# Kernel tuning notes

Measured on AMD Instinct MI355X. Metric: run time of the kernel, lower is better.

Reference implementation:

```python
import jax, jax.numpy as jnp
import numpy as np

DIM = 1024

def setup_inputs() -> dict:
    key = jax.random.key(0)
    ks = jax.random.split(key, 8)
    B, Sx, Sy, D = 4, 2048, 2048, DIM
    s = 1.0 / np.sqrt(D)
    return {
        "x": jax.random.normal(ks[0], (B, Sx, D), jnp.float32),
        "y": jax.random.normal(ks[1], (B, Sy, D), jnp.float32),
        "Wq": jax.random.normal(ks[2], (D, D), jnp.float32) * s,
        "bq": jnp.zeros((D,), jnp.float32),
        "Wk": jax.random.normal(ks[3], (D, D), jnp.float32) * s,
        "bk": jnp.zeros((D,), jnp.float32),
        "Wv": jax.random.normal(ks[4], (D, D), jnp.float32) * s,
        "bv": jnp.zeros((D,), jnp.float32),
    }

def reference(x, y, Wq, bq, Wk, bk, Wv, bv):
    D = x.shape[-1]
    scale = jnp.sqrt(jnp.asarray(D, x.dtype))
    Q = jnp.einsum('bsd,de->bse', x, Wq) + bq  # [B,Sx,D]
    K = jnp.einsum('btd,de->bte', y, Wk) + bk  # [B,Sy,D]
    V = jnp.einsum('btd,de->bte', y, Wv) + bv  # [B,Sy,D]
    scores = jnp.einsum('bse,bte->bst', Q, K) / scale  # [B,Sx,Sy]
    probs = jax.nn.softmax(scores, axis=-1)
    out = jnp.einsum('bst,bte->bse', probs, V)  # [B,Sx,D]
    return out
```

## Files before the change

### kernel.cpp

```cpp
#include <hip/hip_runtime.h>

typedef __bf16 bf16x8_t __attribute__((ext_vector_type(8)));
typedef float f32x4_t __attribute__((ext_vector_type(4)));
typedef unsigned short ushort_t;

__device__ __forceinline__ unsigned short f2bf(float f) {
  unsigned u = __float_as_uint(f);
  u = (u + 0x7FFFu + ((u >> 16) & 1u)) >> 16;
  return (unsigned short)u;
}
__device__ __forceinline__ float bf2f(unsigned short h) {
  return __uint_as_float(((unsigned)h) << 16);
}

__device__ __forceinline__ void gload16(const void* g, void* l) {
  __builtin_amdgcn_global_load_lds(
      (const __attribute__((address_space(1))) unsigned int*)g,
      (__attribute__((address_space(3))) unsigned int*)l, 16, 0, 0);
}

template<bool OUT_BF16, bool HAS_BIAS>
__global__ __launch_bounds__(256, 3)
void gemm_nt(const ushort_t* __restrict__ A, const ushort_t* __restrict__ Bt,
             void* __restrict__ Cp, const float* __restrict__ bias,
             int gx, int gy, int K, int lda, int ldb, int ldc,
             long sA, long sB, long sC, float alpha)
{
  __shared__ __align__(16) ushort_t smem[2][8192];
  const int tid = threadIdx.x;
  const int lane = tid & 63;
  const int wave = tid >> 6;

  const int per = gridDim.x >> 3;
  int wg = blockIdx.x;
  wg = (wg & 7) * per + (wg >> 3);
  const int bz = wg / (gx * gy);
  const int rr = wg - bz * gx * gy;
  const int by = rr / gx, bx = rr - by * gx;
  const int bm = by * 128, bn = bx * 128;

  const ushort_t* Ab = A + (long)bz * sA;
  const ushort_t* Bb = Bt + (long)bz * sB;

  const int r_s0 = wave * 16 + (lane >> 2);
  const int r_s1 = (wave + 4) * 16 + (lane >> 2);
  const int c_s0 = (((lane & 3) ^ ((r_s0 >> 1) & 3)) << 3);
  const int c_s1 = (((lane & 3) ^ ((r_s1 >> 1) & 3)) << 3);
  const ushort_t* gA0 = Ab + (long)(bm + r_s0) * lda + c_s0;
  const ushort_t* gA1 = Ab + (long)(bm + r_s1) * lda + c_s1;
  const ushort_t* gB0 = Bb + (long)(bn + r_s0) * ldb + c_s0;
  const ushort_t* gB1 = Bb + (long)(bn + r_s1) * ldb + c_s1;

  auto stage = [&](int kt, int buf) {
    const int k0 = kt << 5;
    ushort_t* s = smem[buf];
    gload16(gA0 + k0, s + wave * 512);
    gload16(gA1 + k0, s + (wave + 4) * 512);
    gload16(gB0 + k0, s + 4096 + wave * 512);
    gload16(gB1 + k0, s + 4096 + (wave + 4) * 512);
  };

  const int wr = wave >> 1, wc = wave & 1;
  int offA[4], offB[4];
#pragma unroll
  for (int m = 0; m < 4; ++m) {
    const int row = wr * 64 + m * 16 + (lane & 15);
    offA[m] = row * 32 + ((((lane >> 4) ^ ((row >> 1) & 3))) << 3);
  }
#pragma unroll
  for (int n = 0; n < 4; ++n) {
    const int row = wc * 64 + n * 16 + (lane & 15);
    offB[n] = 4096 + row * 32 + ((((lane >> 4) ^ ((row >> 1) & 3))) << 3);
  }

  f32x4_t acc[4][4];
  const f32x4_t z4 = {0.f, 0.f, 0.f, 0.f};
#pragma unroll
  for (int m = 0; m < 4; ++m)
#pragma unroll
    for (int n = 0; n < 4; ++n) acc[m][n] = z4;

  stage(0, 0);
  __syncthreads();

  const int nt = K >> 5;
  for (int kt = 0; kt < nt; ++kt) {
    const int cur = kt & 1;
    if (kt + 1 < nt) stage(kt + 1, cur ^ 1);
    const ushort_t* s = smem[cur];
    bf16x8_t af[4], bfv[4];
#pragma unroll
    for (int m = 0; m < 4; ++m)
      af[m] = __builtin_bit_cast(bf16x8_t, *(const uint4*)(s + offA[m]));
#pragma unroll
    for (int n = 0; n < 4; ++n)
      bfv[n] = __builtin_bit_cast(bf16x8_t, *(const uint4*)(s + offB[n]));
#pragma unroll
    for (int m = 0; m < 4; ++m)
#pragma unroll
      for (int n = 0; n < 4; ++n)
        acc[m][n] = __builtin_amdgcn_mfma_f32_16x16x32_bf16(af[m], bfv[n], acc[m][n], 0, 0, 0);
    __syncthreads();
  }

  const long zC = (long)bz * sC;
  const int r0 = (lane >> 4) * 4;
  const int c0 = lane & 15;
#pragma unroll
  for (int m = 0; m < 4; ++m) {
    const int grow0 = bm + wr * 64 + m * 16 + r0;
#pragma unroll
    for (int n = 0; n < 4; ++n) {
      const int gcol = bn + wc * 64 + n * 16 + c0;
      float bv_ = 0.f;
      if constexpr (HAS_BIAS) bv_ = bias[gcol];
#pragma unroll
      for (int i = 0; i < 4; ++i) {
        const float v = acc[m][n][i] * alpha + bv_;
        if constexpr (OUT_BF16) {
          ((ushort_t*)Cp)[zC + (long)(grow0 + i) * ldc + gcol] = f2bf(v);
        } else {
          ((float*)Cp)[zC + (long)(grow0 + i) * ldc + gcol] = v;
        }
      }
    }
  }
}

__global__ __launch_bounds__(256)
void conv_f32_bf16(const float* __restrict__ in, ushort_t* __restrict__ out) {
  const long i = (long)blockIdx.x * 256 + threadIdx.x;
  const float4 a = ((const float4*)in)[i * 2];
  const float4 b = ((const float4*)in)[i * 2 + 1];
  uint4 o;
  o.x = (unsigned)f2bf(a.x) | ((unsigned)f2bf(a.y) << 16);
  o.y = (unsigned)f2bf(a.z) | ((unsigned)f2bf(a.w) << 16);
  o.z = (unsigned)f2bf(b.x) | ((unsigned)f2bf(b.y) << 16);
  o.w = (unsigned)f2bf(b.z) | ((unsigned)f2bf(b.w) << 16);
  ((uint4*)out)[i] = o;
}

__global__ __launch_bounds__(256)
void wtrans(const float* __restrict__ W, ushort_t* __restrict__ Wt) {
  __shared__ float tile[32][33];
  const int bx = blockIdx.x * 32;
  const int by = blockIdx.y * 32;
  const int t = threadIdx.x;
  const int c = t & 31, r0 = t >> 5;
#pragma unroll
  for (int i = 0; i < 4; ++i)
    tile[r0 + i * 8][c] = W[(long)(by + r0 + i * 8) * 1024 + bx + c];
  __syncthreads();
#pragma unroll
  for (int i = 0; i < 4; ++i)
    Wt[(long)(bx + r0 + i * 8) * 1024 + by + c] = f2bf(tile[c][r0 + i * 8]);
}

__global__ __launch_bounds__(256)
void transpose_bf16(const ushort_t* __restrict__ in, ushort_t* __restrict__ out,
                    int rows, int cols) {
  __shared__ ushort_t t[64][65];
  in += (long)blockIdx.z * rows * cols;
  out += (long)blockIdx.z * rows * cols;
  const int r0 = blockIdx.y * 64, c0 = blockIdx.x * 64;
  const int tc = threadIdx.x & 31;
  const int tr = threadIdx.x >> 5;
#pragma unroll
  for (int i = 0; i < 8; ++i) {
    const unsigned v = *(const unsigned*)(in + (long)(r0 + tr + 8 * i) * cols + c0 + tc * 2);
    t[tr + 8 * i][tc * 2] = (ushort_t)(v & 0xffff);
    t[tr + 8 * i][tc * 2 + 1] = (ushort_t)(v >> 16);
  }
  __syncthreads();
#pragma unroll
  for (int i = 0; i < 8; ++i) {
    const unsigned v = (unsigned)t[tc * 2][tr + 8 * i] |
                       ((unsigned)t[tc * 2 + 1][tr + 8 * i] << 16);
    *(unsigned*)(out + (long)(c0 + tr + 8 * i) * rows + r0 + tc * 2) = v;
  }
}

__global__ __launch_bounds__(256)
void softmax_rows(ushort_t* __restrict__ S) {
  const long row = blockIdx.x;
  ushort_t* p = S + row * 2048;
  const int t = threadIdx.x;
  uint4 v = ((uint4*)p)[t];
  ushort_t* hp = (ushort_t*)&v;
  float f[8];
#pragma unroll
  for (int j = 0; j < 8; ++j) f[j] = bf2f(hp[j]);

  float m = f[0];
#pragma unroll
  for (int j = 1; j < 8; ++j) m = fmaxf(m, f[j]);
#pragma unroll
  for (int s = 32; s; s >>= 1) m = fmaxf(m, __shfl_xor(m, s, 64));
  __shared__ float redm[4];
  __shared__ float reds[4];
  const int wave = t >> 6, lane = t & 63;
  if (lane == 0) redm[wave] = m;
  __syncthreads();
  m = fmaxf(fmaxf(redm[0], redm[1]), fmaxf(redm[2], redm[3]));

  float sum = 0.f;
#pragma unroll
  for (int j = 0; j < 8; ++j) { f[j] = __expf(f[j] - m); sum += f[j]; }
#pragma unroll
  for (int s = 32; s; s >>= 1) sum += __shfl_xor(sum, s, 64);
  if (lane == 0) reds[wave] = sum;
  __syncthreads();
  sum = reds[0] + reds[1] + reds[2] + reds[3];
  const float inv = 1.0f / sum;
#pragma unroll
  for (int j = 0; j < 8; ++j) hp[j] = f2bf(f[j] * inv);
  ((uint4*)p)[t] = v;
}

extern "C" void kernel_launch(void* const* d_in, const int* in_sizes, int n_in,
                              void* d_out, int out_size, void* d_ws, size_t ws_size,
                              hipStream_t stream) {
  const float* x  = (const float*)d_in[0];
  const float* y  = (const float*)d_in[1];
  const float* Wq = (const float*)d_in[2];
  const float* bq = (const float*)d_in[3];
  const float* Wk = (const float*)d_in[4];
  const float* bk = (const float*)d_in[5];
  const float* Wv = (const float*)d_in[6];
  const float* bv = (const float*)d_in[7];
  float* out = (float*)d_out;

  const int B = 4, Sx = 2048, Sy = 2048, D = 1024;
  const long M = (long)B * Sx;

  ushort_t* ws  = (ushort_t*)d_ws;
  ushort_t* Wqt = ws;
  ushort_t* Wkt = Wqt + (1u << 20);
  ushort_t* Wvt = Wkt + (1u << 20);
  ushort_t* Qb  = Wvt + (1u << 20);
  ushort_t* Kb  = Qb + (8u << 20);
  ushort_t* Sb  = Kb + (8u << 20);
  ushort_t* xb  = Sb + (16u << 20);
  ushort_t* yb  = xb + (8u << 20);
  ushort_t* Vn  = Sb;
  ushort_t* Vt  = xb;

  dim3 blk(256);

  conv_f32_bf16<<<dim3(4096), blk, 0, stream>>>(x, xb);
  conv_f32_bf16<<<dim3(4096), blk, 0, stream>>>(y, yb);
  wtrans<<<dim3(32, 32), blk, 0, stream>>>(Wq, Wqt);
  wtrans<<<dim3(32, 32), blk, 0, stream>>>(Wk, Wkt);
  wtrans<<<dim3(32, 32), blk, 0, stream>>>(Wv, Wvt);

  gemm_nt<true, true><<<dim3(512), blk, 0, stream>>>(
      xb, Wqt, Qb, bq, 8, 64, D, D, D, D, 0, 0, 0, 1.0f);
  gemm_nt<true, true><<<dim3(512), blk, 0, stream>>>(
      yb, Wkt, Kb, bk, 8, 64, D, D, D, D, 0, 0, 0, 1.0f);
  gemm_nt<true, true><<<dim3(512), blk, 0, stream>>>(
      yb, Wvt, Vn, bv, 8, 64, D, D, D, D, 0, 0, 0, 1.0f);
  transpose_bf16<<<dim3(16, 32, 4), blk, 0, stream>>>(Vn, Vt, Sy, D);

  gemm_nt<true, false><<<dim3(1024), blk, 0, stream>>>(
      Qb, Kb, Sb, nullptr, 16, 16, D, D, D, Sy,
      (long)Sx * D, (long)Sy * D, (long)Sx * Sy, 0.03125f);

  softmax_rows<<<dim3(B * Sx), blk, 0, stream>>>(Sb);

  gemm_nt<false, false><<<dim3(512), blk, 0, stream>>>(
      Sb, Vt, out, nullptr, 8, 16, Sy, Sy, Sy, D,
      (long)Sx * Sy, (long)D * Sy, (long)Sx * D, 1.0f);
}
```

Measured before the change: 208.3 us.

## Switch GEMMs to 32x32x16 MFMA, fuse K/V projection, batch prep kernels

The GEMM kernel now uses 32x32x16 bf16 MFMA with 2x2 accumulator tiles per wave in place of 4x4 tiles of 16x16x32, with a matching LDS swizzle and a launch bound of 4. The K and V projections become one GEMM over concatenated weights and biases, writing interleaved KV rows, so y is read once. The f32-to-bf16 conversion and the three weight transposes are merged into single launches. The goal is fewer LDS reads per MFMA and fewer kernel launches. The cost is a strided epilogue layout and an extra small bias-concat kernel.

After: 217.3 us. 4.3% more time.

```diff
diff --git a/kernel.cpp b/kernel.cpp
--- a/kernel.cpp
+++ b/kernel.cpp
@@ -1,7 +1,7 @@
 #include <hip/hip_runtime.h>
 
 typedef __bf16 bf16x8_t __attribute__((ext_vector_type(8)));
-typedef float f32x4_t __attribute__((ext_vector_type(4)));
+typedef float f32x16_t __attribute__((ext_vector_type(16)));
 typedef unsigned short ushort_t;
 
 __device__ __forceinline__ unsigned short f2bf(float f) {
@@ -20,16 +20,17 @@
 }
 
 template<bool OUT_BF16, bool HAS_BIAS>
-__global__ __launch_bounds__(256, 3)
-void gemm_nt(const ushort_t* __restrict__ A, const ushort_t* __restrict__ Bt,
-             void* __restrict__ Cp, const float* __restrict__ bias,
-             int gx, int gy, int K, int lda, int ldb, int ldc,
-             long sA, long sB, long sC, float alpha)
+__global__ __launch_bounds__(256, 4)
+void gemm32(const ushort_t* __restrict__ A, const ushort_t* __restrict__ Bt,
+            void* __restrict__ Cp, const float* __restrict__ bias,
+            int gx, int gy, int K, int lda, int ldb, int ldc,
+            long sA, long sB, long sC, float alpha)
 {
-  __shared__ __align__(16) ushort_t smem[2][8192];
+  __shared__ __align__(16) ushort_t sm[16384];
   const int tid = threadIdx.x;
   const int lane = tid & 63;
-  const int wave = tid >> 6;
+  const int w = tid >> 6;
+  const int wr = w >> 1, wc = w & 1;
 
   const int per = gridDim.x >> 3;
   int wg = blockIdx.x;
@@ -39,88 +40,94 @@
   const int by = rr / gx, bx = rr - by * gx;
   const int bm = by * 128, bn = bx * 128;
 
-  const ushort_t* Ab = A + (long)bz * sA;
-  const ushort_t* Bb = Bt + (long)bz * sB;
-
-  const int r_s0 = wave * 16 + (lane >> 2);
-  const int r_s1 = (wave + 4) * 16 + (lane >> 2);
-  const int c_s0 = (((lane & 3) ^ ((r_s0 >> 1) & 3)) << 3);
-  const int c_s1 = (((lane & 3) ^ ((r_s1 >> 1) & 3)) << 3);
-  const ushort_t* gA0 = Ab + (long)(bm + r_s0) * lda + c_s0;
-  const ushort_t* gA1 = Ab + (long)(bm + r_s1) * lda + c_s1;
-  const ushort_t* gB0 = Bb + (long)(bn + r_s0) * ldb + c_s0;
-  const ushort_t* gB1 = Bb + (long)(bn + r_s1) * ldb + c_s1;
+  const int r0 = (w * 2) * 16 + (lane >> 2);
+  const int csw = (((lane & 3) ^ (r0 & 3)) << 3);
+  const ushort_t* pA0 = A + (long)bz * sA + (long)(bm + r0) * lda + csw;
+  const ushort_t* pA1 = pA0 + 16 * lda;
+  const ushort_t* pB0 = Bt + (long)bz * sB + (long)(bn + r0) * ldb + csw;
+  const ushort_t* pB1 = pB0 + 16 * ldb;
 
   auto stage = [&](int kt, int buf) {
     const int k0 = kt << 5;
-    ushort_t* s = smem[buf];
-    gload16(gA0 + k0, s + wave * 512);
-    gload16(gA1 + k0, s + (wave + 4) * 512);
-    gload16(gB0 + k0, s + 4096 + wave * 512);
-    gload16(gB1 + k0, s + 4096 + (wave + 4) * 512);
+    ushort_t* s = sm + buf * 8192;
+    gload16(pA0 + k0, s + (w * 2) * 512);
+    gload16(pA1 + k0, s + (w * 2 + 1) * 512);
+    gload16(pB0 + k0, s + 4096 + (w * 2) * 512);
+    gload16(pB1 + k0, s + 4096 + (w * 2 + 1) * 512);
   };
 
-  const int wr = wave >> 1, wc = wave & 1;
-  int offA[4], offB[4];
-#pragma unroll
-  for (int m = 0; m < 4; ++m) {
-    const int row = wr * 64 + m * 16 + (lane & 15);
-    offA[m] = row * 32 + ((((lane >> 4) ^ ((row >> 1) & 3))) << 3);
-  }
-#pragma unroll
-  for (int n = 0; n < 4; ++n) {
-    const int row = wc * 64 + n * 16 + (lane & 15);
-    offB[n] = 4096 + row * 32 + ((((lane >> 4) ^ ((row >> 1) & 3))) << 3);
-  }
-
-  f32x4_t acc[4][4];
-  const f32x4_t z4 = {0.f, 0.f, 0.f, 0.f};
-#pragma unroll
-  for (int m = 0; m < 4; ++m)
-#pragma unroll
-    for (int n = 0; n < 4; ++n) acc[m][n] = z4;
+  const int l31 = lane & 31, kh = lane >> 5;
+  int offA[2][2], offB[2][2];
+#pragma unroll
+  for (int m = 0; m < 2; ++m) {
+    const int row = wr * 64 + m * 32 + l31;
+#pragma unroll
+    for (int s = 0; s < 2; ++s)
+      offA[m][s] = row * 32 + (((s * 2 + kh) ^ (row & 3)) << 3);
+  }
+#pragma unroll
+  for (int n = 0; n < 2; ++n) {
+    const int row = wc * 64 + n * 32 + l31;
+#pragma unroll
+    for (int s = 0; s < 2; ++s)
+      offB[n][s] = 4096 + row * 32 + (((s * 2 + kh) ^ (row & 3)) << 3);
+  }
+
+  f32x16_t acc[2][2];
+#pragma unroll
+  for (int m = 0; m < 2; ++m)
+#pragma unroll
+    for (int n = 0; n < 2; ++n)
+#pragma unroll
+      for (int i = 0; i < 16; ++i) acc[m][n][i] = 0.f;
 
   stage(0, 0);
   __syncthreads();
 
+#define LDX(off) __builtin_bit_cast(bf16x8_t, *(const uint4*)(sp + (off)))
   const int nt = K >> 5;
   for (int kt = 0; kt < nt; ++kt) {
     const int cur = kt & 1;
     if (kt + 1 < nt) stage(kt + 1, cur ^ 1);
-    const ushort_t* s = smem[cur];
-    bf16x8_t af[4], bfv[4];
-#pragma unroll
-    for (int m = 0; m < 4; ++m)
-      af[m] = __builtin_bit_cast(bf16x8_t, *(const uint4*)(s + offA[m]));
-#pragma unroll
-    for (int n = 0; n < 4; ++n)
-      bfv[n] = __builtin_bit_cast(bf16x8_t, *(const uint4*)(s + offB[n]));
-#pragma unroll
-    for (int m = 0; m < 4; ++m)
-#pragma unroll
-      for (int n = 0; n < 4; ++n)
-        acc[m][n] = __builtin_amdgcn_mfma_f32_16x16x32_bf16(af[m], bfv[n], acc[m][n], 0, 0, 0);
+    const ushort_t* sp = sm + cur * 8192;
+    bf16x8_t af[2][2], bf[2][2];
+#pragma unroll
+    for (int m = 0; m < 2; ++m)
+#pragma unroll
+      for (int s = 0; s < 2; ++s) af[m][s] = LDX(offA[m][s]);
+#pragma unroll
+    for (int n = 0; n < 2; ++n)
+#pragma unroll
+      for (int s = 0; s < 2; ++s) bf[n][s] = LDX(offB[n][s]);
+#pragma unroll
+    for (int s = 0; s < 2; ++s)
+#pragma unroll
+      for (int m = 0; m < 2; ++m)
+#pragma unroll
+        for (int n = 0; n < 2; ++n)
+          acc[m][n] = __builtin_amdgcn_mfma_f32_32x32x16_bf16(
+              af[m][s], bf[n][s], acc[m][n], 0, 0, 0);
     __syncthreads();
   }
+#undef LDX
 
   const long zC = (long)bz * sC;
-  const int r0 = (lane >> 4) * 4;
-  const int c0 = lane & 15;
-#pragma unroll
-  for (int m = 0; m < 4; ++m) {
-    const int grow0 = bm + wr * 64 + m * 16 + r0;
-#pragma unroll
-    for (int n = 0; n < 4; ++n) {
-      const int gcol = bn + wc * 64 + n * 16 + c0;
+#pragma unroll
+  for (int m = 0; m < 2; ++m) {
+    const int growb = bm + wr * 64 + m * 32;
+#pragma unroll
+    for (int n = 0; n < 2; ++n) {
+      const int gcol = bn + wc * 64 + n * 32 + l31;
       float bv_ = 0.f;
       if constexpr (HAS_BIAS) bv_ = bias[gcol];
 #pragma unroll
-      for (int i = 0; i < 4; ++i) {
-        const float v = acc[m][n][i] * alpha + bv_;
+      for (int r = 0; r < 16; ++r) {
+        const int grow = growb + (r & 3) + 8 * (r >> 2) + 4 * kh;
+        const float v = acc[m][n][r] * alpha + bv_;
         if constexpr (OUT_BF16) {
-          ((ushort_t*)Cp)[zC + (long)(grow0 + i) * ldc + gcol] = f2bf(v);
+          ((ushort_t*)Cp)[zC + (long)grow * ldc + gcol] = f2bf(v);
         } else {
-          ((float*)Cp)[zC + (long)(grow0 + i) * ldc + gcol] = v;
+          ((float*)Cp)[zC + (long)grow * ldc + gcol] = v;
         }
       }
     }
@@ -128,20 +135,28 @@
 }
 
 __global__ __launch_bounds__(256)
-void conv_f32_bf16(const float* __restrict__ in, ushort_t* __restrict__ out) {
-  const long i = (long)blockIdx.x * 256 + threadIdx.x;
+void conv2(const float* __restrict__ x, const float* __restrict__ y,
+           ushort_t* __restrict__ xb, ushort_t* __restrict__ yb) {
+  const int b = blockIdx.x;
+  const float* in = (b < 4096) ? x : y;
+  ushort_t* out = (b < 4096) ? xb : yb;
+  const long i = (long)(b & 4095) * 256 + threadIdx.x;
   const float4 a = ((const float4*)in)[i * 2];
-  const float4 b = ((const float4*)in)[i * 2 + 1];
+  const float4 c = ((const float4*)in)[i * 2 + 1];
   uint4 o;
   o.x = (unsigned)f2bf(a.x) | ((unsigned)f2bf(a.y) << 16);
   o.y = (unsigned)f2bf(a.z) | ((unsigned)f2bf(a.w) << 16);
-  o.z = (unsigned)f2bf(b.x) | ((unsigned)f2bf(b.y) << 16);
-  o.w = (unsigned)f2bf(b.z) | ((unsigned)f2bf(b.w) << 16);
+  o.z = (unsigned)f2bf(c.x) | ((unsigned)f2bf(c.y) << 16);
+  o.w = (unsigned)f2bf(c.z) | ((unsigned)f2bf(c.w) << 16);
   ((uint4*)out)[i] = o;
 }
 
 __global__ __launch_bounds__(256)
-void wtrans(const float* __restrict__ W, ushort_t* __restrict__ Wt) {
+void wtrans3(const float* __restrict__ W0, const float* __restrict__ W1,
+             const float* __restrict__ W2, ushort_t* __restrict__ T0,
+             ushort_t* __restrict__ T1, ushort_t* __restrict__ T2) {
+  const float* W = (blockIdx.z == 0) ? W0 : (blockIdx.z == 1) ? W1 : W2;
+  ushort_t* Wt = (blockIdx.z == 0) ? T0 : (blockIdx.z == 1) ? T1 : T2;
   __shared__ float tile[32][33];
   const int bx = blockIdx.x * 32;
   const int by = blockIdx.y * 32;
@@ -157,26 +172,33 @@
 }
 
 __global__ __launch_bounds__(256)
+void bconcat(const float* __restrict__ a, const float* __restrict__ b,
+             float* __restrict__ o) {
+  const int i = blockIdx.x * 256 + threadIdx.x;
+  o[i] = (i < 1024) ? a[i] : b[i - 1024];
+}
+
+__global__ __launch_bounds__(256)
 void transpose_bf16(const ushort_t* __restrict__ in, ushort_t* __restrict__ out,
-                    int rows, int cols) {
-  __shared__ ushort_t t[64][65];
-  in += (long)blockIdx.z * rows * cols;
-  out += (long)blockIdx.z * rows * cols;
+                    int ld_in, int ld_out, long in_bs, long out_bs) {
+  __shared__ ushort_t tt[64][65];
+  in += (long)blockIdx.z * in_bs;
+  out += (long)blockIdx.z * out_bs;
   const int r0 = blockIdx.y * 64, c0 = blockIdx.x * 64;
   const int tc = threadIdx.x & 31;
   const int tr = threadIdx.x >> 5;
 #pragma unroll
   for (int i = 0; i < 8; ++i) {
-    const unsigned v = *(const unsigned*)(in + (long)(r0 + tr + 8 * i) * cols + c0 + tc * 2);
-    t[tr + 8 * i][tc * 2] = (ushort_t)(v & 0xffff);
-    t[tr + 8 * i][tc * 2 + 1] = (ushort_t)(v >> 16);
+    const unsigned v = *(const unsigned*)(in + (long)(r0 + tr + 8 * i) * ld_in + c0 + tc * 2);
+    tt[tr + 8 * i][tc * 2] = (ushort_t)(v & 0xffff);
+    tt[tr + 8 * i][tc * 2 + 1] = (ushort_t)(v >> 16);
   }
   __syncthreads();
 #pragma unroll
   for (int i = 0; i < 8; ++i) {
-    const unsigned v = (unsigned)t[tc * 2][tr + 8 * i] |
-                       ((unsigned)t[tc * 2 + 1][tr + 8 * i] << 16);
-    *(unsigned*)(out + (long)(c0 + tr + 8 * i) * rows + r0 + tc * 2) = v;
+    const unsigned v = (unsigned)tt[tc * 2][tr + 8 * i] |
+                       ((unsigned)tt[tc * 2 + 1][tr + 8 * i] << 16);
+    *(unsigned*)(out + (long)(c0 + tr + 8 * i) * ld_out + r0 + tc * 2) = v;
   }
 }
 
@@ -230,44 +252,41 @@
   const float* bv = (const float*)d_in[7];
   float* out = (float*)d_out;
 
-  const int B = 4, Sx = 2048, Sy = 2048, D = 1024;
-  const long M = (long)B * Sx;
+  const int D = 1024;
+  const long MB_ = 1l << 20;
 
   ushort_t* ws  = (ushort_t*)d_ws;
   ushort_t* Wqt = ws;
-  ushort_t* Wkt = Wqt + (1u << 20);
-  ushort_t* Wvt = Wkt + (1u << 20);
-  ushort_t* Qb  = Wvt + (1u << 20);
-  ushort_t* Kb  = Qb + (8u << 20);
-  ushort_t* Sb  = Kb + (8u << 20);
-  ushort_t* xb  = Sb + (16u << 20);
-  ushort_t* yb  = xb + (8u << 20);
-  ushort_t* Vn  = Sb;
-  ushort_t* Vt  = xb;
+  ushort_t* Wkv = ws + 1 * MB_;
+  ushort_t* Wvt = ws + 2 * MB_;
+  ushort_t* Qb  = ws + 3 * MB_;
+  ushort_t* KV  = ws + 11 * MB_;
+  ushort_t* yb  = ws + 27 * MB_;
+  ushort_t* Vt  = ws + 27 * MB_;
+  ushort_t* xb  = ws + 35 * MB_;
+  ushort_t* Sb  = ws + 35 * MB_;
+  float*    bkv = (float*)(ws + 51 * MB_);
 
   dim3 blk(256);
 
-  conv_f32_bf16<<<dim3(4096), blk, 0, stream>>>(x, xb);
-  conv_f32_bf16<<<dim3(4096), blk, 0, stream>>>(y, yb);
-  wtrans<<<dim3(32, 32), blk, 0, stream>>>(Wq, Wqt);
-  wtrans<<<dim3(32, 32), blk, 0, stream>>>(Wk, Wkt);
-  wtrans<<<dim3(32, 32), blk, 0, stream>>>(Wv, Wvt);
-
-  gemm_nt<true, true><<<dim3(512), blk, 0, stream>>>(
+  conv2<<<dim3(8192), blk, 0, stream>>>(x, y, xb, yb);
+  wtrans3<<<dim3(32, 32, 3), blk, 0, stream>>>(Wq, Wk, Wv, Wqt, Wkv, Wvt);
+  bconcat<<<dim3(8), blk, 0, stream>>>(bk, bv, bkv);
+
+  gemm32<true, true><<<dim3(512), blk, 0, stream>>>(
       xb, Wqt, Qb, bq, 8, 64, D, D, D, D, 0, 0, 0, 1.0f);
-  gemm_nt<true, true><<<dim3(512), blk, 0, stream>>>(
-      yb, Wkt, Kb, bk, 8, 64, D, D, D, D, 0, 0, 0, 1.0f);
-  gemm_nt<true, true><<<dim3(512), blk, 0, stream>>>(
-      yb, Wvt, Vn, bv, 8, 64, D, D, D, D, 0, 0, 0, 1.0f);
-  transpose_bf16<<<dim3(16, 32, 4), blk, 0, stream>>>(Vn, Vt, Sy, D);
-
-  gemm_nt<true, false><<<dim3(1024), blk, 0, stream>>>(
-      Qb, Kb, Sb, nullptr, 16, 16, D, D, D, Sy,
-      (long)Sx * D, (long)Sy * D, (long)Sx * Sy, 0.03125f);
-
-  softmax_rows<<<dim3(B * Sx), blk, 0, stream>>>(Sb);
-
-  gemm_nt<false, false><<<dim3(512), blk, 0, stream>>>(
-      Sb, Vt, out, nullptr, 8, 16, Sy, Sy, Sy, D,
-      (long)Sx * Sy, (long)D * Sy, (long)Sx * D, 1.0f);
-}
+  gemm32<true, true><<<dim3(1024), blk, 0, stream>>>(
+      yb, Wkv, KV, bkv, 16, 64, D, D, D, 2048, 0, 0, 0, 1.0f);
+  transpose_bf16<<<dim3(16, 32, 4), blk, 0, stream>>>(
+      KV + 1024, Vt, 2048, 2048, 2048l * 2048, 1024l * 2048);
+
+  gemm32<true, false><<<dim3(1024), blk, 0, stream>>>(
+      Qb, KV, Sb, nullptr, 16, 16, D, D, 2048, 2048,
+      2048l * 1024, 2048l * 2048, 2048l * 2048, 0.03125f);
+
+  softmax_rows<<<dim3(8192), blk, 0, stream>>>(Sb);
+
+  gemm32<false, false><<<dim3(512), blk, 0, stream>>>(
+      Sb, Vt, out, nullptr, 8, 16, 2048, 2048, 2048, D,
+      2048l * 2048, 1024l * 2048, 2048l * 1024, 1.0f);
+}
```
